# Kernel optimization log

Measured on AMD Instinct MI355X. Metric: run time of the kernel, lower is better.

The kernel has to match this reference:

```python
import jax, jax.numpy as jnp
import numpy as np

N_PER_BATCH = 65536
BATCH = 4
N = N_PER_BATCH * BATCH
C = 64
GS = 64
HEADS = 4
ORDER = 10
GRID = (512, 512, 64)


def hilbert_encode(xyz, order):
    """Skilling's AxesToTranspose + bit interleave. xyz: [M,3] int -> [M] int64 codes."""
    X = [xyz[:, i].astype(jnp.int64) for i in range(3)]
    M = 1 << (order - 1)
    Q = M
    while Q > 1:  # inverse-undo
        P = Q - 1
        for i in range(3):
            cond = (X[i] & Q) != 0
            if i == 0:
                X[0] = jnp.where(cond, X[0] ^ P, X[0])
            else:
                t = (X[0] ^ X[i]) & P
                x0 = jnp.where(cond, X[0] ^ P, X[0] ^ t)
                xi = jnp.where(cond, X[i], X[i] ^ t)
                X[0], X[i] = x0, xi
        Q >>= 1
    for i in range(1, 3):  # gray encode
        X[i] = X[i] ^ X[i - 1]
    t = jnp.zeros_like(X[0])
    Q = M
    while Q > 1:
        t = jnp.where((X[2] & Q) != 0, t ^ (Q - 1), t)
        Q >>= 1
    X = [x ^ t for x in X]
    code = jnp.zeros_like(X[0])
    for b in range(order - 1, -1, -1):  # interleave transposed bits -> hilbert index
        for i in range(3):
            code = (code << 1) | ((X[i] >> b) & 1)
    return code


def batched_codes(coors, order):
    # batch index in high bits keeps each cloud contiguous after the global argsort
    return (coors[:, 0].astype(jnp.int64) << (3 * order)) | hilbert_encode(coors[:, 1:], order)


def inv_perm(p):
    return jnp.zeros_like(p).at[p].set(jnp.arange(p.shape[0], dtype=p.dtype))


def mapping(vox_coors, order):
    # MULTI_GROUP == 'shift': second grouping shifts the last two spatial coords by 1
    coors2 = jnp.concatenate([vox_coors[:, :2], vox_coors[:, 2:] + 1], axis=-1)
    ind1 = jnp.argsort(batched_codes(vox_coors, order))
    ind2 = jnp.argsort(batched_codes(coors2, order))
    inv1, inv2 = inv_perm(ind1), inv_perm(ind2)
    ind12 = inv1[ind2]  # reindex: order-1-sorted -> order-2-sorted
    ind21 = inv2[ind1]  # reindex: order-2-sorted -> order-1-sorted
    return ind1, ind2, ind12, ind21


def layernorm(x):
    m = jnp.mean(x, -1, keepdims=True)
    v = jnp.var(x, -1, keepdims=True)
    return (x - m) * jax.lax.rsqrt(v + 1e-5)


def vox_block(p, x, w_pos, w_qkv, w_o, w_ffa, w_ffb, gs, heads):
    """VoxFormer layer: grouped (window) attention over contiguous groups of size gs."""
    c = x.shape[-1]
    hd = c // heads
    x = x + p @ w_pos                       # inject point coords
    qkv = layernorm(x) @ w_qkv              # [N, 3C]
    g = x.shape[0] // gs
    q, k, v = [a.reshape(g, gs, heads, hd) for a in jnp.split(qkv, 3, axis=-1)]
    att = jax.nn.softmax(jnp.einsum('gqhd,gkhd->ghqk', q, k) * (1.0 / float(np.sqrt(hd))), axis=-1)
    o = jnp.einsum('ghqk,gkhd->gqhd', att, v).reshape(-1, c)
    x = x + o @ w_o
    x = x + jax.nn.gelu(layernorm(x) @ w_ffa) @ w_ffb
    return x


def setup_inputs():
    key = jax.random.key(0)
    ks = jax.random.split(key, 16)
    vox_feats = jax.random.normal(ks[0], (N, C), jnp.float32)
    pts_coors = jax.random.normal(ks[1], (N, 4), jnp.float32)
    bidx = jnp.repeat(jnp.arange(BATCH, dtype=jnp.int32), N_PER_BATCH)[:, None]
    xyz = jnp.stack([jax.random.randint(ks[2 + i], (N,), 0, GRID[i], jnp.int32) for i in range(3)], -1)
    vox_coors = jnp.concatenate([bidx, xyz], -1)
    vox_numbs = jnp.full((BATCH,), N_PER_BATCH, jnp.int32)
    s = 0.02
    params = {
        'w_pos1': jax.random.normal(ks[5], (4, C), jnp.float32) * s,
        'w_qkv1': jax.random.normal(ks[6], (C, 3 * C), jnp.float32) * s,
        'w_o1': jax.random.normal(ks[7], (C, C), jnp.float32) * s,
        'w_ffa1': jax.random.normal(ks[8], (C, 4 * C), jnp.float32) * s,
        'w_ffb1': jax.random.normal(ks[9], (4 * C, C), jnp.float32) * s,
        'w_pos2': jax.random.normal(ks[10], (4, C), jnp.float32) * s,
        'w_qkv2': jax.random.normal(ks[11], (C, 3 * C), jnp.float32) * s,
        'w_o2': jax.random.normal(ks[12], (C, C), jnp.float32) * s,
        'w_ffa2': jax.random.normal(ks[13], (C, 4 * C), jnp.float32) * s,
        'w_ffb2': jax.random.normal(ks[14], (4 * C, C), jnp.float32) * s,
    }
    return dict(vox_feats=vox_feats, pts_coors=pts_coors, vox_coors=vox_coors,
                vox_numbs=vox_numbs, group_size=GS, order=ORDER, **params)


def reference(vox_feats, pts_coors, vox_coors, vox_numbs, group_size, order,
              w_pos1, w_qkv1, w_o1, w_ffa1, w_ffb1,
              w_pos2, w_qkv2, w_o2, w_ffa2, w_ffb2):
    ind1, ind2, ind12, ind21 = mapping(vox_coors, order)
    blocks = [(w_pos1, w_qkv1, w_o1, w_ffa1, w_ffb1),
              (w_pos2, w_qkv2, w_o2, w_ffa2, w_ffb2)]
    ind_list = [ind1] + [ind12, ind21] * (len(blocks) // 2)
    for ind, bw in zip(ind_list, blocks):
        vox_feats = vox_feats[ind]
        pts_coors = pts_coors[ind]
        vox_coors = vox_coors[ind]
        vox_feats = vox_block(pts_coors, vox_feats, *bw, group_size, HEADS)
    return vox_feats
```

## Files before the change

kernel.cpp:

```cpp
#include <hip/hip_runtime.h>
#include <hip/hip_bf16.h>
#include <math.h>

#define NTOT 262144
#define SEG 65536

typedef unsigned short u16;
typedef unsigned int u32;
typedef unsigned long long u64;
typedef __attribute__((ext_vector_type(4))) float f32x4;
typedef __attribute__((ext_vector_type(8))) short s16x8;

__device__ __forceinline__ float bf2f(u32 lo16) { return __uint_as_float(lo16 << 16); }
__device__ __forceinline__ u16 cvt_bf16(float f) {
  return __builtin_bit_cast(u16, __float2bfloat16(f));
}
__device__ __forceinline__ u32 cvt_bf16x2(float a, float b) {
  return (u32)cvt_bf16(a) | ((u32)cvt_bf16(b) << 16);
}

__device__ __forceinline__ float fast_exp2(float x) {
#if __has_builtin(__builtin_amdgcn_exp2f)
  return __builtin_amdgcn_exp2f(x);
#else
  return __expf(x * 0.69314718056f);
#endif
}
__device__ __forceinline__ float fast_rcp(float x) {
#if __has_builtin(__builtin_amdgcn_rcpf)
  return __builtin_amdgcn_rcpf(x);
#else
  return 1.f / x;
#endif
}

__device__ __forceinline__ unsigned int hilbert10(unsigned int X0, unsigned int X1, unsigned int X2) {
#pragma unroll
  for (unsigned int Q = 512u; Q > 1u; Q >>= 1) {
    unsigned int P = Q - 1u;
    X0 ^= (X0 & Q) ? P : 0u;
    {
      unsigned int t = (X0 ^ X1) & P;
      bool c = (X1 & Q) != 0u;
      X0 ^= c ? P : t;
      X1 ^= c ? 0u : t;
    }
    {
      unsigned int t = (X0 ^ X2) & P;
      bool c = (X2 & Q) != 0u;
      X0 ^= c ? P : t;
      X2 ^= c ? 0u : t;
    }
  }
  X1 ^= X0;
  X2 ^= X1;
  unsigned int t = 0u;
#pragma unroll
  for (unsigned int Q = 512u; Q > 1u; Q >>= 1) t ^= (X2 & Q) ? (Q - 1u) : 0u;
  X0 ^= t; X1 ^= t; X2 ^= t;
  unsigned int code = 0u;
#pragma unroll
  for (int b = 9; b >= 0; b--) {
    code = (code << 3) | (((X0 >> b) & 1u) << 2) | (((X1 >> b) & 1u) << 1) | ((X2 >> b) & 1u);
  }
  return code;
}

__global__ __launch_bounds__(1024) void k_bitonic_local4k(
    const int* __restrict__ coors, u64* __restrict__ keys,
    const float* __restrict__ wq1, const float* __restrict__ wo1,
    const float* __restrict__ wa1, const float* __restrict__ wb1,
    const float* __restrict__ wq2, const float* __restrict__ wo2,
    const float* __restrict__ wa2, const float* __restrict__ wb2,
    u16* __restrict__ wpk) {
  const int tid = threadIdx.x;
  const int slice = blockIdx.y;
  const int tile = blockIdx.x;
  const int seg = slice & 3;
  const int arr = slice >> 2;
  const int rbase = (seg ^ 2) * SEG + tile * 4096;
  const int tbase = tile * 4096;
  __shared__ u64 s[4096];

  for (int i = tid; i < 4096; i += 1024) {
    int r = rbase + i;
    int4 cc = ((const int4*)coors)[r];
    u32 code = arr == 0
        ? hilbert10((unsigned)cc.y, (unsigned)cc.z, (unsigned)cc.w)
        : hilbert10((unsigned)cc.y, (unsigned)(cc.z + 1), (unsigned)(cc.w + 1));
    s[i] = ((u64)code << 18) | (u64)(u32)r;
  }
  if (slice == 0) {
    int gtid = tile * 1024 + tid;
    if (gtid < 12288) {
      int b = gtid >> 6;
      int set = b >= 96;
      int f = b - set * 96;
      const float* W; int nt, ks, N, off;
      if (f < 24)      { W = set ? wq2 : wq1; nt = f >> 1;        ks = f & 1;        N = 192; off = 0     + f * 512; }
      else if (f < 32) { W = set ? wo2 : wo1; nt = (f - 24) >> 1; ks = (f - 24) & 1; N = 64;  off = 12288 + (f - 24) * 512; }
      else if (f < 64) { W = set ? wa2 : wa1; nt = (f - 32) >> 1; ks = (f - 32) & 1; N = 256; off = 16384 + (f - 32) * 512; }
      else             { W = set ? wb2 : wb1; nt = (f - 64) >> 3; ks = (f - 64) & 7; N = 64;  off = 32768 + (f - 64) * 512; }
      int l = gtid & 63;
      int n = nt * 16 + (l & 15);
      int k0 = ks * 32 + (l >> 4) * 8;
      u16* o = wpk + (size_t)set * 49152 + off + l * 8;
#pragma unroll
      for (int i = 0; i < 8; i++) o[i] = cvt_bf16(W[(size_t)(k0 + i) * N + n]);
    }
  }
  __syncthreads();

  for (int k = 2; k <= 4096; k <<= 1) {
    for (int j = k >> 1; j > 0; j >>= 1) {
      for (int p = tid; p < 2048; p += 1024) {
        int i = ((p & ~(j - 1)) << 1) | (p & (j - 1));
        int ix = i | j;
        bool asc = (((tbase + i) & k) == 0);
        u64 x = s[i], y = s[ix];
        if ((x > y) == asc) { s[i] = y; s[ix] = x; }
      }
      __syncthreads();
    }
  }
  u64* a = keys + (size_t)slice * SEG + tbase;
  for (int i = tid; i < 4096; i += 1024) a[i] = s[i];
}

__global__ __launch_bounds__(256) void k_bitonic_global(u64* __restrict__ keys,
                                                        int k, int j) {
  u64* a = keys + (size_t)blockIdx.y * SEG;
  int p = blockIdx.x * 256 + threadIdx.x;
  int i = ((p & ~(j - 1)) << 1) | (p & (j - 1));
  int ix = i | j;
  bool asc = ((i & k) == 0);
  u64 x = a[i], y = a[ix];
  if ((x > y) == asc) { a[i] = y; a[ix] = x; }
}

__global__ __launch_bounds__(256) void k_bitonic_g2(u64* __restrict__ keys,
                                                    int k, int j) {
  u64* a = keys + (size_t)blockIdx.y * SEG;
  int p = blockIdx.x * 256 + threadIdx.x;
  int jl = j >> 1;
  int i0 = ((p & ~(jl - 1)) << 2) | (p & (jl - 1));
  bool asc = ((i0 & k) == 0);
  u64 a0 = a[i0], a1 = a[i0 + jl], a2 = a[i0 + j], a3 = a[i0 + j + jl];
  if ((a0 > a2) == asc) { u64 t = a0; a0 = a2; a2 = t; }
  if ((a1 > a3) == asc) { u64 t = a1; a1 = a3; a3 = t; }
  if ((a0 > a1) == asc) { u64 t = a0; a0 = a1; a1 = t; }
  if ((a2 > a3) == asc) { u64 t = a2; a2 = a3; a3 = t; }
  a[i0] = a0; a[i0 + jl] = a1; a[i0 + j] = a2; a[i0 + j + jl] = a3;
}

__global__ __launch_bounds__(1024) void k_bitonic_finish4k(
    u64* __restrict__ keys, int k, int last,
    int* __restrict__ ind1, int* __restrict__ ind2, int* __restrict__ inv1) {
  const int tid = threadIdx.x;
  const int slice = blockIdx.y;
  const int tile = blockIdx.x;
  const int tbase = tile * 4096;
  u64* a = keys + (size_t)slice * SEG + tbase;
  __shared__ u64 s[4096];
  for (int i = tid; i < 4096; i += 1024) s[i] = a[i];
  __syncthreads();
  bool asc = ((tbase & k) == 0);
  for (int j = 2048; j > 0; j >>= 1) {
    for (int p = tid; p < 2048; p += 1024) {
      int i = ((p & ~(j - 1)) << 1) | (p & (j - 1));
      int ix = i | j;
      u64 x = s[i], y = s[ix];
      if ((x > y) == asc) { s[i] = y; s[ix] = x; }
    }
    __syncthreads();
  }
  if (!last) {
    for (int i = tid; i < 4096; i += 1024) a[i] = s[i];
  } else {
    for (int i = tid; i < 4096; i += 1024) {
      int p = tbase + i;
      int e = (int)(s[i] & 0x3FFFFULL);
      if (slice < 4) {
        int gr = slice * SEG + p;
        ind1[gr] = e;
        inv1[e] = gr;
      } else {
        ind2[(slice - 4) * SEG + p] = e;
      }
    }
  }
}

__device__ __forceinline__ float gelu_tanh(float v) {
  float t = v * v;
  float u = fmaf(t, -0.1029433f, -2.3022081f);
  float e = fast_exp2(u * v);
  return v * fast_rcp(1.f + e);
}

__device__ __forceinline__ int l144(int row, int byte) { return row * 144 + byte; }
__device__ __forceinline__ int l272(int row, int byte) { return row * 272 + byte; }

#define MFMA(A, B, C) __builtin_amdgcn_mfma_f32_16x16x32_bf16(A, B, C, 0, 0, 0)

__global__ __launch_bounds__(256, 4) void k_block(
    const float* __restrict__ srcF, const u16* __restrict__ srcB,
    const float* __restrict__ pts,
    const int* __restrict__ indF, const int* __restrict__ indP,
    const int* __restrict__ remap,
    const float* __restrict__ w_pos, const u16* __restrict__ wpk,
    u16* __restrict__ outB, float* __restrict__ outF) {
  __shared__ __align__(16) char lds_qk[64 * 272];
  __shared__ __align__(16) char lds_vT[64 * 144];

  const int tid = threadIdx.x;
  const int l = tid & 63;
  const int w = tid >> 6;
  const int c4 = l >> 4;
  const int ln = l & 15;
  const int base = blockIdx.x * 64;
  char* qkB = lds_qk;
  char* vtB = lds_vT;
  char* oB = lds_vT;

  f32x4 xv[4];
#pragma unroll
  for (int reg = 0; reg < 4; reg++) {
    int r = base + w * 16 + c4 * 4 + reg;
    int iF = indF[r];
    if (remap) iF = remap[iF];
    int iP = indP[r];
    float4 pc = ((const float4*)pts)[iP];
#pragma unroll
    for (int nt = 0; nt < 4; nt++) {
      int col = ln + nt * 16;
      float v = srcB ? bf2f(srcB[(size_t)iF * 64 + col]) : srcF[(size_t)iF * 64 + col];
      v += pc.x * w_pos[col] + pc.y * w_pos[64 + col] + pc.z * w_pos[128 + col] + pc.w * w_pos[192 + col];
      xv[nt][reg] = v;
    }
  }
#pragma unroll
  for (int reg = 0; reg < 4; reg++) {
    float s = xv[0][reg] + xv[1][reg] + xv[2][reg] + xv[3][reg];
    float s2 = xv[0][reg] * xv[0][reg] + xv[1][reg] * xv[1][reg]
             + xv[2][reg] * xv[2][reg] + xv[3][reg] * xv[3][reg];
#pragma unroll
    for (int m = 1; m <= 8; m <<= 1) { s += __shfl_xor(s, m, 64); s2 += __shfl_xor(s2, m, 64); }
    float mean = s * 0.015625f;
    float rs = rsqrtf(s2 * 0.015625f - mean * mean + 1e-5f);
    int rl = c4 * 4 + reg;
#pragma unroll
    for (int nt = 0; nt < 4; nt++)
      *(u16*)(qkB + l272(w * 16 + rl, nt * 32 + ln * 2)) = cvt_bf16((xv[nt][reg] - mean) * rs);
  }
  s16x8 la0 = *(const s16x8*)(qkB + l272(w * 16 + ln, c4 * 16));
  s16x8 la1 = *(const s16x8*)(qkB + l272(w * 16 + ln, 64 + c4 * 16));

  const uint4* wq = (const uint4*)wpk;
#pragma unroll 4
  for (int nt = 0; nt < 12; nt++) {
    s16x8 b0 = *(const s16x8*)(wq + (nt * 2 + 0) * 64 + l);
    s16x8 b1 = *(const s16x8*)(wq + (nt * 2 + 1) * 64 + l);
    f32x4 c = {0.f, 0.f, 0.f, 0.f};
    c = MFMA(la0, b0, c);
    c = MFMA(la1, b1, c);
    if (nt < 8) {
      int bib = nt * 32 + ln * 2;
#pragma unroll
      for (int reg = 0; reg < 4; reg++)
        *(u16*)(qkB + l272(w * 16 + c4 * 4 + reg, bib)) = cvt_bf16(c[reg]);
    } else {
      int vrow = (nt - 8) * 16 + ln;
      uint2 pk = make_uint2(cvt_bf16x2(c[0], c[1]), cvt_bf16x2(c[2], c[3]));
      *(uint2*)(vtB + l144(vrow, w * 32 + c4 * 8)) = pk;
    }
  }
  __syncthreads();

  const int h = w;
  const s16x8 z8 = {0, 0, 0, 0, 0, 0, 0, 0};
  s16x8 kb[4], vb[2];
#pragma unroll
  for (int nt = 0; nt < 4; nt++) {
    s16x8 t = *(const s16x8*)(qkB + l272(nt * 16 + ln, 128 + h * 32 + (c4 & 1) * 16));
    kb[nt] = (c4 < 2) ? t : z8;
  }
#pragma unroll
  for (int ks = 0; ks < 2; ks++)
    vb[ks] = *(const s16x8*)(vtB + l144(h * 16 + ln, ks * 64 + c4 * 16));
  __syncthreads();
#pragma unroll 1
  for (int mt = 0; mt < 4; mt++) {
    s16x8 qa = *(const s16x8*)(qkB + l272(mt * 16 + ln, h * 32 + (c4 & 1) * 16));
    if (c4 >= 2) qa = z8;
    f32x4 sv[4];
#pragma unroll
    for (int nt = 0; nt < 4; nt++) {
      f32x4 c = {0.f, 0.f, 0.f, 0.f};
      sv[nt] = MFMA(qa, kb[nt], c);
    }
    float invr[4];
#pragma unroll
    for (int reg = 0; reg < 4; reg++) {
      float p0 = fast_exp2(sv[0][reg] * 0.3606737602f);
      float p1 = fast_exp2(sv[1][reg] * 0.3606737602f);
      float p2 = fast_exp2(sv[2][reg] * 0.3606737602f);
      float p3 = fast_exp2(sv[3][reg] * 0.3606737602f);
      float sum = p0 + p1 + p2 + p3;
#pragma unroll
      for (int m = 1; m <= 8; m <<= 1) sum += __shfl_xor(sum, m, 64);
      invr[reg] = fast_rcp(sum);
      int rl = c4 * 4 + reg;
      *(u16*)(qkB + l272(w * 16 + rl, 128 + 0 * 32 + ln * 2)) = cvt_bf16(p0);
      *(u16*)(qkB + l272(w * 16 + rl, 128 + 1 * 32 + ln * 2)) = cvt_bf16(p1);
      *(u16*)(qkB + l272(w * 16 + rl, 128 + 2 * 32 + ln * 2)) = cvt_bf16(p2);
      *(u16*)(qkB + l272(w * 16 + rl, 128 + 3 * 32 + ln * 2)) = cvt_bf16(p3);
    }
    s16x8 pa0 = *(const s16x8*)(qkB + l272(w * 16 + ln, 128 + c4 * 16));
    s16x8 pa1 = *(const s16x8*)(qkB + l272(w * 16 + ln, 128 + 64 + c4 * 16));
    f32x4 o = {0.f, 0.f, 0.f, 0.f};
    o = MFMA(pa0, vb[0], o);
    o = MFMA(pa1, vb[1], o);
#pragma unroll
    for (int reg = 0; reg < 4; reg++)
      *(u16*)(oB + l144(mt * 16 + c4 * 4 + reg, h * 32 + ln * 2)) = cvt_bf16(o[reg] * invr[reg]);
  }
  __syncthreads();

  s16x8 oa0 = *(const s16x8*)(oB + l144(w * 16 + ln, c4 * 16));
  s16x8 oa1 = *(const s16x8*)(oB + l144(w * 16 + ln, 64 + c4 * 16));
  const uint4* wo = (const uint4*)(wpk + 12288);
  f32x4 x2[4];
#pragma unroll
  for (int nt = 0; nt < 4; nt++) {
    s16x8 b0 = *(const s16x8*)(wo + (nt * 2 + 0) * 64 + l);
    s16x8 b1 = *(const s16x8*)(wo + (nt * 2 + 1) * 64 + l);
    f32x4 c = xv[nt];
    c = MFMA(oa0, b0, c);
    c = MFMA(oa1, b1, c);
    x2[nt] = c;
  }

#pragma unroll
  for (int reg = 0; reg < 4; reg++) {
    float s = x2[0][reg] + x2[1][reg] + x2[2][reg] + x2[3][reg];
    float s2 = x2[0][reg] * x2[0][reg] + x2[1][reg] * x2[1][reg]
             + x2[2][reg] * x2[2][reg] + x2[3][reg] * x2[3][reg];
#pragma unroll
    for (int m = 1; m <= 8; m <<= 1) { s += __shfl_xor(s, m, 64); s2 += __shfl_xor(s2, m, 64); }
    float mean = s * 0.015625f;
    float rs = rsqrtf(s2 * 0.015625f - mean * mean + 1e-5f);
    int rl = c4 * 4 + reg;
#pragma unroll
    for (int nt = 0; nt < 4; nt++)
      *(u16*)(qkB + l272(w * 16 + rl, nt * 32 + ln * 2)) = cvt_bf16((x2[nt][reg] - mean) * rs);
  }
  s16x8 fa0 = *(const s16x8*)(qkB + l272(w * 16 + ln, c4 * 16));
  s16x8 fa1 = *(const s16x8*)(qkB + l272(w * 16 + ln, 64 + c4 * 16));
  const uint4* wfa = (const uint4*)(wpk + 16384);
  const uint4* wfb = (const uint4*)(wpk + 32768);
  f32x4 acc[4];
#pragma unroll
  for (int nt = 0; nt < 4; nt++) acc[nt] = x2[nt];
#pragma unroll 1
  for (int rd = 0; rd < 4; rd++) {
#pragma unroll
    for (int t = 0; t < 4; t++) {
      int nt = rd * 4 + t;
      s16x8 b0 = *(const s16x8*)(wfa + (nt * 2 + 0) * 64 + l);
      s16x8 b1 = *(const s16x8*)(wfa + (nt * 2 + 1) * 64 + l);
      f32x4 hc = {0.f, 0.f, 0.f, 0.f};
      hc = MFMA(fa0, b0, hc);
      hc = MFMA(fa1, b1, hc);
#pragma unroll
      for (int reg = 0; reg < 4; reg++)
        *(u16*)(qkB + l272(w * 16 + c4 * 4 + reg, 128 + t * 32 + ln * 2)) = cvt_bf16(gelu_tanh(hc[reg]));
    }
    s16x8 ha0 = *(const s16x8*)(qkB + l272(w * 16 + ln, 128 + c4 * 16));
    s16x8 ha1 = *(const s16x8*)(qkB + l272(w * 16 + ln, 128 + 64 + c4 * 16));
#pragma unroll
    for (int nt = 0; nt < 4; nt++) {
      s16x8 b0 = *(const s16x8*)(wfb + (nt * 8 + rd * 2 + 0) * 64 + l);
      s16x8 b1 = *(const s16x8*)(wfb + (nt * 8 + rd * 2 + 1) * 64 + l);
      acc[nt] = MFMA(ha0, b0, acc[nt]);
      acc[nt] = MFMA(ha1, b1, acc[nt]);
    }
  }

#pragma unroll
  for (int reg = 0; reg < 4; reg++) {
    size_t r = (size_t)(base + w * 16 + c4 * 4 + reg) * 64;
#pragma unroll
    for (int nt = 0; nt < 4; nt++) {
      size_t idx = r + ln + nt * 16;
      if (outB) outB[idx] = cvt_bf16(acc[nt][reg]);
      else outF[idx] = acc[nt][reg];
    }
  }
}

extern "C" void kernel_launch(void* const* d_in, const int* in_sizes, int n_in,
                              void* d_out, int out_size, void* d_ws, size_t ws_size,
                              hipStream_t stream) {
  const float* vox_feats = (const float*)d_in[0];
  const float* pts = (const float*)d_in[1];
  const int* coors = (const int*)d_in[2];
  const float* w_pos1 = (const float*)d_in[6];
  const float* w_qkv1 = (const float*)d_in[7];
  const float* w_o1 = (const float*)d_in[8];
  const float* w_ffa1 = (const float*)d_in[9];
  const float* w_ffb1 = (const float*)d_in[10];
  const float* w_pos2 = (const float*)d_in[11];
  const float* w_qkv2 = (const float*)d_in[12];
  const float* w_o2 = (const float*)d_in[13];
  const float* w_ffa2 = (const float*)d_in[14];
  const float* w_ffb2 = (const float*)d_in[15];

  char* ws = (char*)d_ws;
  int* ind1 = (int*)ws;
  int* ind2 = ind1 + NTOT;
  int* inv1 = ind2 + NTOT;
  u64* keys = (u64*)(ws + ((size_t)4 << 20));
  u16* f1 = (u16*)(ws + ((size_t)8 << 20));
  u16* wpk = (u16*)(ws + ((size_t)40 << 20));
  float* outp = (float*)d_out;

  k_bitonic_local4k<<<dim3(SEG / 4096, 8), 1024, 0, stream>>>(
      coors, keys, w_qkv1, w_o1, w_ffa1, w_ffb1, w_qkv2, w_o2, w_ffa2, w_ffb2, wpk);
  for (int k = 8192; k <= SEG; k <<= 1) {
    int j = k >> 1;
    while (j >= 8192) {
      k_bitonic_g2<<<dim3(SEG / 1024, 8), 256, 0, stream>>>(keys, k, j);
      j >>= 2;
    }
    if (j == 4096) {
      k_bitonic_global<<<dim3(SEG / 512, 8), 256, 0, stream>>>(keys, k, 4096);
    }
    k_bitonic_finish4k<<<dim3(SEG / 4096, 8), 1024, 0, stream>>>(
        keys, k, (k == SEG) ? 1 : 0, ind1, ind2, inv1);
  }

  k_block<<<NTOT / 64, 256, 0, stream>>>(vox_feats, (const u16*)nullptr, pts,
                                         ind1, ind1, (const int*)nullptr,
                                         w_pos1, wpk, f1, (float*)nullptr);
  k_block<<<NTOT / 64, 256, 0, stream>>>((const float*)nullptr, f1, pts,
                                         ind2, ind2, inv1,
                                         w_pos2, wpk + 49152,
                                         (u16*)nullptr, outp);
}
```

Measured before the change: 414.4 us.

## Enlarge shared-memory bitonic finish tile to 8K and add radix-8 global pass

The bitonic sort's shared-memory finishing kernel now handles 8192-element tiles instead of 4096, so more merge stages stay in LDS. A new radix-8 global kernel fuses three compare-exchange stages per pass. The merge schedule is unrolled into a fixed launch sequence. Together these cut the number of kernel launches and global memory round trips over the keys. The cost is 64KB of shared memory per block, which lowers occupancy.

```diff
diff --git a/kernel.cpp b/kernel.cpp
--- a/kernel.cpp
+++ b/kernel.cpp
@@ -153,20 +153,45 @@
   a[i0] = a0; a[i0 + jl] = a1; a[i0 + j] = a2; a[i0 + j + jl] = a3;
 }
 
-__global__ __launch_bounds__(1024) void k_bitonic_finish4k(
+__global__ __launch_bounds__(256) void k_bitonic_g3(u64* __restrict__ keys,
+                                                    int k, int j) {
+  u64* a = keys + (size_t)blockIdx.y * SEG;
+  int p = blockIdx.x * 256 + threadIdx.x;
+  int q = j >> 2;
+  int i0 = ((p & ~(q - 1)) << 3) | (p & (q - 1));
+  bool asc = ((i0 & k) == 0);
+  u64 v[8];
+#pragma unroll
+  for (int m = 0; m < 8; m++) v[m] = a[i0 + m * q];
+#pragma unroll
+  for (int m = 0; m < 4; m++)
+    if ((v[m] > v[m + 4]) == asc) { u64 t = v[m]; v[m] = v[m + 4]; v[m + 4] = t; }
+#pragma unroll
+  for (int h = 0; h < 8; h += 4)
+#pragma unroll
+    for (int m = 0; m < 2; m++)
+      if ((v[h + m] > v[h + m + 2]) == asc) { u64 t = v[h + m]; v[h + m] = v[h + m + 2]; v[h + m + 2] = t; }
+#pragma unroll
+  for (int h = 0; h < 8; h += 2)
+    if ((v[h] > v[h + 1]) == asc) { u64 t = v[h]; v[h] = v[h + 1]; v[h + 1] = t; }
+#pragma unroll
+  for (int m = 0; m < 8; m++) a[i0 + m * q] = v[m];
+}
+
+__global__ __launch_bounds__(1024) void k_bitonic_finish8k(
     u64* __restrict__ keys, int k, int last,
     int* __restrict__ ind1, int* __restrict__ ind2, int* __restrict__ inv1) {
   const int tid = threadIdx.x;
   const int slice = blockIdx.y;
   const int tile = blockIdx.x;
-  const int tbase = tile * 4096;
+  const int tbase = tile * 8192;
   u64* a = keys + (size_t)slice * SEG + tbase;
-  __shared__ u64 s[4096];
-  for (int i = tid; i < 4096; i += 1024) s[i] = a[i];
+  __shared__ u64 s[8192];
+  for (int i = tid; i < 8192; i += 1024) s[i] = a[i];
   __syncthreads();
   bool asc = ((tbase & k) == 0);
-  for (int j = 2048; j > 0; j >>= 1) {
-    for (int p = tid; p < 2048; p += 1024) {
+  for (int j = 4096; j > 0; j >>= 1) {
+    for (int p = tid; p < 4096; p += 1024) {
       int i = ((p & ~(j - 1)) << 1) | (p & (j - 1));
       int ix = i | j;
       u64 x = s[i], y = s[ix];
@@ -175,9 +200,9 @@
     __syncthreads();
   }
   if (!last) {
-    for (int i = tid; i < 4096; i += 1024) a[i] = s[i];
+    for (int i = tid; i < 8192; i += 1024) a[i] = s[i];
   } else {
-    for (int i = tid; i < 4096; i += 1024) {
+    for (int i = tid; i < 8192; i += 1024) {
       int p = tbase + i;
       int e = (int)(s[i] & 0x3FFFFULL);
       if (slice < 4) {
@@ -427,18 +452,17 @@
 
   k_bitonic_local4k<<<dim3(SEG / 4096, 8), 1024, 0, stream>>>(
       coors, keys, w_qkv1, w_o1, w_ffa1, w_ffb1, w_qkv2, w_o2, w_ffa2, w_ffb2, wpk);
-  for (int k = 8192; k <= SEG; k <<= 1) {
-    int j = k >> 1;
-    while (j >= 8192) {
-      k_bitonic_g2<<<dim3(SEG / 1024, 8), 256, 0, stream>>>(keys, k, j);
-      j >>= 2;
-    }
-    if (j == 4096) {
-      k_bitonic_global<<<dim3(SEG / 512, 8), 256, 0, stream>>>(keys, k, 4096);
-    }
-    k_bitonic_finish4k<<<dim3(SEG / 4096, 8), 1024, 0, stream>>>(
-        keys, k, (k == SEG) ? 1 : 0, ind1, ind2, inv1);
-  }
+  k_bitonic_finish8k<<<dim3(SEG / 8192, 8), 1024, 0, stream>>>(
+      keys, 8192, 0, ind1, ind2, inv1);
+  k_bitonic_global<<<dim3(SEG / 512, 8), 256, 0, stream>>>(keys, 16384, 8192);
+  k_bitonic_finish8k<<<dim3(SEG / 8192, 8), 1024, 0, stream>>>(
+      keys, 16384, 0, ind1, ind2, inv1);
+  k_bitonic_g2<<<dim3(SEG / 1024, 8), 256, 0, stream>>>(keys, 32768, 16384);
+  k_bitonic_finish8k<<<dim3(SEG / 8192, 8), 1024, 0, stream>>>(
+      keys, 32768, 0, ind1, ind2, inv1);
+  k_bitonic_g3<<<dim3(SEG / 2048, 8), 256, 0, stream>>>(keys, 65536, 32768);
+  k_bitonic_finish8k<<<dim3(SEG / 8192, 8), 1024, 0, stream>>>(
+      keys, 65536, 1, ind1, ind2, inv1);
 
   k_block<<<NTOT / 64, 256, 0, stream>>>(vox_feats, (const u16*)nullptr, pts,
                                          ind1, ind1, (const int*)nullptr,
```

Result: slower. 423.8 us (+2.3%).
